# Performance work log

Measured on AMD Instinct MI355X. Metric: run time of the kernel, lower is better.

Reference implementation:

```python
import jax, jax.numpy as jnp
import numpy as np

B, T, D, H, L, INNER = 2, 2048, 1024, 16, 8, 4096
EPS = 1e-5
MASK_BIAS = -10000.0

def setup_inputs() -> dict:
    key = jax.random.key(0)
    ks = jax.random.split(key, 6)
    std = 0.02
    w = lambda k, shape: jax.random.normal(k, shape, jnp.float32) * std
    return {
        "inputs_embeds": jax.random.normal(ks[0], (B, T, D), jnp.float32),
        "attention_mask": jnp.ones((B, T), jnp.float32),
        "ln1_w": jnp.ones((L, D), jnp.float32), "ln1_b": jnp.zeros((L, D), jnp.float32),
        "attn_w": w(ks[1], (L, D, 3 * D)), "attn_b": jnp.zeros((L, 3 * D), jnp.float32),
        "proj_w": w(ks[2], (L, D, D)), "proj_b": jnp.zeros((L, D), jnp.float32),
        "ln2_w": jnp.ones((L, D), jnp.float32), "ln2_b": jnp.zeros((L, D), jnp.float32),
        "fc_w": w(ks[3], (L, D, INNER)), "fc_b": jnp.zeros((L, INNER), jnp.float32),
        "fcp_w": w(ks[4], (L, INNER, D)), "fcp_b": jnp.zeros((L, D), jnp.float32),
        "lnf_w": jnp.ones((D,), jnp.float32), "lnf_b": jnp.zeros((D,), jnp.float32),
    }

def _ln(x, w, b):
    m = jnp.mean(x, axis=-1, keepdims=True)
    v = jnp.var(x, axis=-1, keepdims=True)
    return (x - m) * jax.lax.rsqrt(v + EPS) * w + b

def reference(inputs_embeds, attention_mask, ln1_w, ln1_b, attn_w, attn_b,
              proj_w, proj_b, ln2_w, ln2_b, fc_w, fc_b, fcp_w, fcp_b,
              lnf_w, lnf_b):
    hd = D // H
    scale = 1.0 / np.sqrt(hd).astype(np.float32)
    causal = jnp.tril(jnp.ones((T, T), bool))            # [T,T]
    add_mask = (1.0 - attention_mask)[:, None, None, :] * MASK_BIAS  # [B,1,1,T]
    heads = lambda t: t.reshape(B, T, H, hd).transpose(0, 2, 1, 3)   # [B,H,T,hd]
    h = inputs_embeds  # dropout is identity at eval
    for i in range(L):
        # --- causal self-attention (manual QK^T / softmax / AV) ---
        x = _ln(h, ln1_w[i], ln1_b[i])
        qkv = x @ attn_w[i] + attn_b[i]                  # [B,T,3D]
        q, k, v = (heads(t) for t in jnp.split(qkv, 3, axis=-1))
        s = jnp.einsum('bhqd,bhkd->bhqk', q, k) * scale  # [B,H,T,T]
        s = jnp.where(causal, s, MASK_BIAS) + add_mask   # masked_fill then additive mask
        p = jax.nn.softmax(s, axis=-1)
        ctx = jnp.einsum('bhqk,bhkd->bhqd', p, v)
        ctx = ctx.transpose(0, 2, 1, 3).reshape(B, T, D)
        h = h + ctx @ proj_w[i] + proj_b[i]
        # --- feed-forward ---
        x = _ln(h, ln2_w[i], ln2_b[i])
        h = h + jax.nn.relu(x @ fc_w[i] + fc_b[i]) @ fcp_w[i] + fcp_b[i]
    return _ln(h, lnf_w, lnf_b)
```

## Files before the change

### kernel.cpp

```cpp
#include <hip/hip_runtime.h>
#include <math.h>

namespace {
constexpr int kB = 2;
constexpr int kT = 2048;
constexpr int kD = 1024;
constexpr int kH = 16;
constexpr int kL = 8;
constexpr int kInner = 4096;
constexpr int kM = kB * kT;
constexpr float kEps = 1e-5f;
}

typedef __attribute__((ext_vector_type(8))) short bf16x8;
typedef __attribute__((ext_vector_type(4))) float f32x4;
typedef __attribute__((ext_vector_type(16))) float f32x16;

typedef const __attribute__((address_space(1))) void* gas_t;
typedef __attribute__((address_space(3))) void* las_t;

__device__ __forceinline__ short f2bf(float f) {
  union { float f; unsigned u; } v{f};
  unsigned r = (v.u + 0x7FFF + ((v.u >> 16) & 1)) >> 16;
  return (short)r;
}

__device__ __forceinline__ unsigned cvtpk_bf16(float lo, float hi) {
  unsigned r;
  asm("v_cvt_pk_bf16_f32 %0, %1, %2" : "=v"(r) : "v"(lo), "v"(hi));
  return r;
}

__device__ __forceinline__ void half_swap(unsigned& a, unsigned& b, bool ishi) {
  const unsigned sel = ishi ? a : b;
  const unsigned got = (unsigned)__shfl_xor((int)sel, 32, 64);
  a = ishi ? got : a;
  b = ishi ? b : got;
}

template <typename OT>
__global__ __launch_bounds__(256) void ln_kernel(
    const float* __restrict__ in, const float* __restrict__ w,
    const float* __restrict__ b, OT* __restrict__ out) {
  const int row = blockIdx.x;
  const int tid = threadIdx.x;
  const float4 v = ((const float4*)(in + (size_t)row * kD))[tid];
  float sum = v.x + v.y + v.z + v.w;
  float sq = v.x * v.x + v.y * v.y + v.z * v.z + v.w * v.w;
#pragma unroll
  for (int off = 32; off > 0; off >>= 1) {
    sum += __shfl_down(sum, off);
    sq += __shfl_down(sq, off);
  }
  __shared__ float s1[4], s2[4];
  const int wave = tid >> 6, lane = tid & 63;
  if (lane == 0) { s1[wave] = sum; s2[wave] = sq; }
  __syncthreads();
  const float ts = s1[0] + s1[1] + s1[2] + s1[3];
  const float tq = s2[0] + s2[1] + s2[2] + s2[3];
  const float mean = ts * (1.0f / kD);
  const float var = tq * (1.0f / kD) - mean * mean;
  const float rs = rsqrtf(var + kEps);
  const float4 w4 = ((const float4*)w)[tid];
  const float4 b4 = ((const float4*)b)[tid];
  float4 o;
  o.x = (v.x - mean) * rs * w4.x + b4.x;
  o.y = (v.y - mean) * rs * w4.y + b4.y;
  o.z = (v.z - mean) * rs * w4.z + b4.z;
  o.w = (v.w - mean) * rs * w4.w + b4.w;
  if constexpr (sizeof(OT) == 4) {
    ((float4*)(out + (size_t)row * kD))[tid] = o;
  } else {
    short4 s4;
    s4.x = f2bf(o.x); s4.y = f2bf(o.y); s4.z = f2bf(o.z); s4.w = f2bf(o.w);
    ((short4*)(out + (size_t)row * kD))[tid] = s4;
  }
}

__global__ __launch_bounds__(256) void convT_kernel(
    const float* __restrict__ aw, const float* __restrict__ pw,
    const float* __restrict__ fw, const float* __restrict__ gw,
    short* __restrict__ awT, short* __restrict__ pwT,
    short* __restrict__ fwT, short* __restrict__ gwT) {
  __shared__ short t[64][66];
  int b = blockIdx.x;
  const float* src; short* dst; int K, N, tk, tn;
  if (b < 768)       { src = aw; dst = awT; K = 1024; N = 3072; tk = b / 48; tn = b % 48; }
  else if (b < 1024) { b -= 768;  src = pw; dst = pwT; K = 1024; N = 1024; tk = b / 16; tn = b % 16; }
  else if (b < 2048) { b -= 1024; src = fw; dst = fwT; K = 1024; N = 4096; tk = b / 64; tn = b % 64; }
  else               { b -= 2048; src = gw; dst = gwT; K = 4096; N = 1024; tk = b / 16; tn = b % 16; }
  const int k0 = tk * 64, n0 = tn * 64;
  const int tr = threadIdx.x >> 4, tc4 = (threadIdx.x & 15) << 2;
#pragma unroll
  for (int i = 0; i < 4; ++i) {
    const int k = tr + i * 16;
    const float4 v = *(const float4*)(src + (size_t)(k0 + k) * N + n0 + tc4);
    t[k][tc4 + 0] = f2bf(v.x); t[k][tc4 + 1] = f2bf(v.y);
    t[k][tc4 + 2] = f2bf(v.z); t[k][tc4 + 3] = f2bf(v.w);
  }
  __syncthreads();
#pragma unroll
  for (int i = 0; i < 4; ++i) {
    const int n = tr + i * 16;
    short4 o;
    o.x = t[tc4 + 0][n]; o.y = t[tc4 + 1][n];
    o.z = t[tc4 + 2][n]; o.w = t[tc4 + 3][n];
    *(short4*)(dst + (size_t)(n0 + n) * K + k0 + tc4) = o;
  }
}

template <int BN_, int OUT, bool RELU>
__global__ __launch_bounds__(256, 4) void mfma_gemm3(
    const short* __restrict__ A, const short* __restrict__ BT,
    const float* __restrict__ bias, const float* __restrict__ res,
    void* __restrict__ Cout, int N, int K) {
  constexpr int NJ = BN_ / 32;
  __shared__ __align__(16) short As[128 * 64];
  __shared__ __align__(16) short Bs[BN_ * 64];
  const int tid = threadIdx.x;
  const int w = tid >> 6, lane = tid & 63;
  const int n16 = lane & 15, quad = lane >> 4;
  const int gridN = N / BN_;
  int bid = blockIdx.x;
  const int nwg = gridDim.x;
  bid = (bid & 7) * (nwg >> 3) + (bid >> 3);
  const int m0 = (bid / gridN) * 128, n0 = (bid % gridN) * BN_;
  const int wr = (w >> 1) * 64, wc = (w & 1) * (BN_ / 2);

  const short* Ap = A + (size_t)m0 * K;
  const short* Bp = BT + (size_t)n0 * K;

  f32x4 acc[4][NJ];
#pragma unroll
  for (int i = 0; i < 4; ++i)
#pragma unroll
    for (int j = 0; j < NJ; ++j) acc[i][j] = (f32x4)0.f;

  const int srow = tid >> 3;
  const int schunk = tid & 7;

  for (int k0 = 0; k0 < K; k0 += 64) {
#pragma unroll
    for (int i = 0; i < 4; ++i) {
      const int r = i * 32 + srow;
      const int cs = (schunk ^ (r & 7)) << 3;
      __builtin_amdgcn_global_load_lds(
          (gas_t)(const void*)(Ap + (size_t)r * K + k0 + cs),
          (las_t)(void*)(As + (i * 32 + w * 8) * 64), 16, 0, 0);
      if (i < NJ)
        __builtin_amdgcn_global_load_lds(
            (gas_t)(const void*)(Bp + (size_t)r * K + k0 + cs),
            (las_t)(void*)(Bs + (i * 32 + w * 8) * 64), 16, 0, 0);
    }
    __syncthreads();

    bf16x8 af[4][2], bf[NJ][2];
#pragma unroll
    for (int i = 0; i < 4; ++i) {
      const int m = wr + i * 16 + n16;
#pragma unroll
      for (int kc = 0; kc < 2; ++kc)
        af[i][kc] =
            *(const bf16x8*)(As + m * 64 + ((((kc << 2) + quad) ^ (m & 7)) << 3));
    }
#pragma unroll
    for (int j = 0; j < NJ; ++j) {
      const int n = wc + j * 16 + n16;
#pragma unroll
      for (int kc = 0; kc < 2; ++kc)
        bf[j][kc] =
            *(const bf16x8*)(Bs + n * 64 + ((((kc << 2) + quad) ^ (n & 7)) << 3));
    }
#pragma unroll
    for (int i = 0; i < 4; ++i)
#pragma unroll
      for (int j = 0; j < NJ; ++j)
#pragma unroll
        for (int kc = 0; kc < 2; ++kc)
          acc[i][j] = __builtin_amdgcn_mfma_f32_16x16x32_bf16(af[i][kc], bf[j][kc],
                                                              acc[i][j], 0, 0, 0);
    __syncthreads();
  }

#pragma unroll
  for (int j = 0; j < NJ; ++j) {
    const int n = n0 + wc + j * 16 + n16;
    const float bv = bias[n];
#pragma unroll
    for (int i = 0; i < 4; ++i) {
#pragma unroll
      for (int r = 0; r < 4; ++r) {
        const int m = m0 + wr + i * 16 + quad * 4 + r;
        float v = acc[i][j][r] + bv;
        if (OUT == 1) {
          ((float*)Cout)[(size_t)m * N + n] = v + res[(size_t)m * N + n];
        } else {
          if (RELU) v = fmaxf(v, 0.f);
          ((short*)Cout)[(size_t)m * N + n] = f2bf(v);
        }
      }
    }
  }
}

__global__ __launch_bounds__(256) void attn_kernel(
    const short* __restrict__ qkv, const float* __restrict__ amaskp,
    short* __restrict__ ctx) {
  __shared__ __align__(16) short smem[2][8192];

  const int tid = threadIdx.x;
  const int w = tid >> 6;
  const int lane = tid & 63;
  const int l31 = lane & 31;
  const int hi = lane >> 5;
  const int bh = blockIdx.x;
  const int bb = bh >> 4, hh = bh & 15;
  const int qb = gridDim.y - 1 - blockIdx.y;
  const int q0 = qb * 128;
  const int qw0 = q0 + w * 32;

  const short* base  = qkv + (size_t)bb * kT * 3072;
  const short* kbase = base + 1024 + hh * 64;
  const short* vbase = base + 2048 + hh * 64;
  const float* amp   = amaskp + bb * kT;

  bf16x8 qf[4];
  {
    const short* qp = base + (size_t)(qw0 + l31) * 3072 + hh * 64 + hi * 8;
#pragma unroll
    for (int mi = 0; mi < 4; ++mi) qf[mi] = *(const bf16x8*)(qp + mi * 16);
  }

  f32x16 O[2];
  O[0] = (f32x16)0.f;
  O[1] = (f32x16)0.f;
  float m_r = -1e30f, l_r = 0.f;

  const int krow = tid >> 3, kch = tid & 7;
  const int vk4 = tid >> 5, vd16 = (tid >> 3) & 3;
  const int vkin = (tid >> 1) & 3, vdh = tid & 1;
  const int wuni = (tid & 192) * 8;

  const unsigned vs0 = (unsigned)(size_t)(las_t)(void*)(&smem[0][4096]);
  const int g = lane >> 4;
  const unsigned vtr =
      vs0 + (unsigned)((g >> 1) * 1024 + (g & 1) * 128 + (lane & 15) * 8);

  auto STAGE = [&](int buf, int k0) {
    short* ks = &smem[buf][0];
    short* vs = &smem[buf][4096];
#pragma unroll
    for (int r2 = 0; r2 < 2; ++r2) {
      const int rr = r2 * 32 + krow;
      __builtin_amdgcn_global_load_lds(
          (gas_t)(const void*)(kbase + (size_t)(k0 + rr) * 3072 +
                               ((kch ^ (rr & 7)) << 3)),
          (las_t)(void*)(ks + r2 * 2048 + wuni), 16, 0, 0);
      const int key = k0 + r2 * 32 + vk4 * 4 + vkin;
      __builtin_amdgcn_global_load_lds(
          (gas_t)(const void*)(vbase + (size_t)key * 3072 + vd16 * 16 + vdh * 8),
          (las_t)(void*)(vs + r2 * 2048 + wuni), 16, 0, 0);
    }
  };

  const int kend = q0 + 128;
  STAGE(0, 0);
  __syncthreads();
  int cur = 0;

  for (int k0 = 0; k0 < kend; k0 += 64) {
    if (k0 + 64 < kend) STAGE(cur ^ 1, k0 + 64);

    if (k0 <= qw0 + 31) {
      const short* ks = &smem[cur][0];

      f32x16 st[2];
      st[0] = (f32x16)0.f;
      st[1] = (f32x16)0.f;
#pragma unroll
      for (int s = 0; s < 2; ++s) {
        const int row = s * 32 + l31;
        const short* kp = ks + row * 64;
#pragma unroll
        for (int mi = 0; mi < 4; ++mi) {
          const bf16x8 kf =
              *(const bf16x8*)(kp + (((2 * mi + hi) ^ (row & 7)) << 3));
          st[s] = __builtin_amdgcn_mfma_f32_32x32x16_bf16(kf, qf[mi], st[s],
                                                          0, 0, 0);
        }
      }

#pragma unroll
      for (int s = 0; s < 2; ++s) {
        const bool pm = (k0 + 32 * s + 31 > qw0);
#pragma unroll
        for (int rq = 0; rq < 4; ++rq) {
          const int kb_ = k0 + 32 * s + 8 * rq + 4 * hi;
          const float4 a4 = *(const float4*)(amp + kb_);
          const float amv0 = (1.f - a4.x) * -10000.f;
          const float amv1 = (1.f - a4.y) * -10000.f;
          const float amv2 = (1.f - a4.z) * -10000.f;
          const float amv3 = (1.f - a4.w) * -10000.f;
          float v0 = st[s][rq * 4 + 0] * 0.125f;
          float v1 = st[s][rq * 4 + 1] * 0.125f;
          float v2 = st[s][rq * 4 + 2] * 0.125f;
          float v3 = st[s][rq * 4 + 3] * 0.125f;
          if (pm) {
            const int q = qw0 + l31;
            if (kb_ + 0 > q) v0 = -10000.f;
            if (kb_ + 1 > q) v1 = -10000.f;
            if (kb_ + 2 > q) v2 = -10000.f;
            if (kb_ + 3 > q) v3 = -10000.f;
          }
          st[s][rq * 4 + 0] = v0 + amv0;
          st[s][rq * 4 + 1] = v1 + amv1;
          st[s][rq * 4 + 2] = v2 + amv2;
          st[s][rq * 4 + 3] = v3 + amv3;
        }
      }

      float mx = st[0][0];
#pragma unroll
      for (int r = 1; r < 16; ++r) mx = fmaxf(mx, st[0][r]);
#pragma unroll
      for (int r = 0; r < 16; ++r) mx = fmaxf(mx, st[1][r]);
      mx = fmaxf(mx, __shfl_xor(mx, 32, 64));
      if (!__all(mx <= m_r + 8.f)) {
        const float mn = fmaxf(m_r, mx);
        const float al = __expf(m_r - mn);
        m_r = mn;
        l_r *= al;
#pragma unroll
        for (int r = 0; r < 16; ++r) {
          O[0][r] *= al;
          O[1][r] *= al;
        }
      }
      float sum = 0.f;
#pragma unroll
      for (int s = 0; s < 2; ++s)
#pragma unroll
        for (int r = 0; r < 16; ++r) {
          const float p = __expf(st[s][r] - m_r);
          st[s][r] = p;
          sum += p;
        }
      sum += __shfl_xor(sum, 32, 64);
      l_r += sum;

      bf16x8 pf[4];
      const bool ishi = (hi != 0);
#pragma unroll
      for (int s = 0; s < 2; ++s) {
#pragma unroll
        for (int hf = 0; hf < 2; ++hf) {
          unsigned wa = cvtpk_bf16(st[s][8 * hf + 0], st[s][8 * hf + 1]);
          unsigned wc = cvtpk_bf16(st[s][8 * hf + 4], st[s][8 * hf + 5]);
          half_swap(wa, wc, ishi);
          unsigned wb = cvtpk_bf16(st[s][8 * hf + 2], st[s][8 * hf + 3]);
          unsigned wd = cvtpk_bf16(st[s][8 * hf + 6], st[s][8 * hf + 7]);
          half_swap(wb, wd, ishi);
          union { unsigned u[4]; bf16x8 h; } f;
          f.u[0] = wa; f.u[1] = wb; f.u[2] = wc; f.u[3] = wd;
          pf[s * 2 + hf] = f.h;
        }
      }

      unsigned long long tv[16];
      const unsigned vb_ = vtr + (unsigned)(cur << 14);
#pragma unroll
      for (int c = 0; c < 4; ++c)
#pragma unroll
        for (int di = 0; di < 2; ++di) {
          asm volatile("ds_read_b64_tr_b16 %0, %1 offset:%2"
                       : "=v"(tv[(c * 2 + di) * 2 + 0])
                       : "v"(vb_), "n"(c * 2048 + di * 256));
          asm volatile("ds_read_b64_tr_b16 %0, %1 offset:%2"
                       : "=v"(tv[(c * 2 + di) * 2 + 1])
                       : "v"(vb_), "n"(c * 2048 + di * 256 + 512));
        }
      asm volatile("s_waitcnt lgkmcnt(0)" ::: "memory");
      __builtin_amdgcn_sched_barrier(0);
#pragma unroll
      for (int c = 0; c < 4; ++c)
#pragma unroll
        for (int di = 0; di < 2; ++di) {
          union { unsigned long long q[2]; bf16x8 h; } vf_;
          vf_.q[0] = tv[(c * 2 + di) * 2 + 0];
          vf_.q[1] = tv[(c * 2 + di) * 2 + 1];
          O[di] = __builtin_amdgcn_mfma_f32_32x32x16_bf16(vf_.h, pf[c], O[di],
                                                          0, 0, 0);
        }
    }

    __syncthreads();
    cur ^= 1;
  }

  const float inv = 1.f / l_r;
  const size_t tok = (size_t)bb * kT + qw0 + l31;
  short* cp = ctx + tok * 1024 + hh * 64 + 4 * hi;
#pragma unroll
  for (int di = 0; di < 2; ++di)
#pragma unroll
    for (int rq = 0; rq < 4; ++rq) {
      short4 o4;
      o4.x = f2bf(O[di][rq * 4 + 0] * inv);
      o4.y = f2bf(O[di][rq * 4 + 1] * inv);
      o4.z = f2bf(O[di][rq * 4 + 2] * inv);
      o4.w = f2bf(O[di][rq * 4 + 3] * inv);
      *(short4*)(cp + di * 32 + rq * 8) = o4;
    }
}

extern "C" void kernel_launch(void* const* d_in, const int* in_sizes, int n_in,
                              void* d_out, int out_size, void* d_ws, size_t ws_size,
                              hipStream_t stream) {
  const float* emb   = (const float*)d_in[0];
  const float* amask = (const float*)d_in[1];
  const float* ln1w  = (const float*)d_in[2];
  const float* ln1b  = (const float*)d_in[3];
  const float* attnw = (const float*)d_in[4];
  const float* attnb = (const float*)d_in[5];
  const float* projw = (const float*)d_in[6];
  const float* projb = (const float*)d_in[7];
  const float* ln2w  = (const float*)d_in[8];
  const float* ln2b  = (const float*)d_in[9];
  const float* fcw   = (const float*)d_in[10];
  const float* fcb   = (const float*)d_in[11];
  const float* fcpw  = (const float*)d_in[12];
  const float* fcpb  = (const float*)d_in[13];
  const float* lnfw  = (const float*)d_in[14];
  const float* lnfb  = (const float*)d_in[15];
  float* out = (float*)d_out;

  float* h    = (float*)d_ws;
  short* xb   = (short*)(h + (size_t)kM * kD);
  short* ctxb = xb + (size_t)kM * kD;
  short* bigb = ctxb + (size_t)kM * kD;
  short* awT  = bigb + (size_t)kM * kInner;
  short* pwT  = awT + (size_t)3072 * 1024;
  short* fwT  = pwT + (size_t)1024 * 1024;
  short* gwT  = fwT + (size_t)4096 * 1024;

  hipMemcpyAsync(h, emb, sizeof(float) * (size_t)kM * kD,
                 hipMemcpyDeviceToDevice, stream);

  const dim3 blk(256);
  for (int l = 0; l < kL; ++l) {
    convT_kernel<<<3072, blk, 0, stream>>>(
        attnw + (size_t)l * kD * 3072, projw + (size_t)l * kD * kD,
        fcw + (size_t)l * kD * kInner, fcpw + (size_t)l * kInner * kD,
        awT, pwT, fwT, gwT);
    ln_kernel<short><<<kM, blk, 0, stream>>>(h, ln1w + l * kD, ln1b + l * kD, xb);
    mfma_gemm3<128, 0, false><<<(3072 / 128) * (kM / 128), blk, 0, stream>>>(
        xb, awT, attnb + l * 3072, nullptr, bigb, 3072, 1024);
    attn_kernel<<<dim3(kB * kH, kT / 128), blk, 0, stream>>>(bigb, amask, ctxb);
    mfma_gemm3<64, 1, false><<<(1024 / 64) * (kM / 128), blk, 0, stream>>>(
        ctxb, pwT, projb + l * kD, h, h, 1024, 1024);
    ln_kernel<short><<<kM, blk, 0, stream>>>(h, ln2w + l * kD, ln2b + l * kD, xb);
    mfma_gemm3<128, 0, true><<<(4096 / 128) * (kM / 128), blk, 0, stream>>>(
        xb, fwT, fcb + l * kInner, nullptr, bigb, 4096, 1024);
    mfma_gemm3<64, 1, false><<<(1024 / 64) * (kM / 128), blk, 0, stream>>>(
        bigb, gwT, fcpb + l * kD, h, h, 1024, 4096);
  }
  ln_kernel<float><<<kM, blk, 0, stream>>>(h, lnfw, lnfb, out);
}
```

Baseline: 2.296 ms.

## Add 256x256 eight-wave pipelined GEMM for QKV and FC1 projections

Adds a new 512-thread GEMM kernel with 256x256 output tiles, double-buffered LDS filled by direct global-to-LDS loads, and a ping-pong schedule that interleaves quarter-tile MFMA blocks with staged loads, barriers and raised wave priority. It also applies an XCD-aware block-id remap so neighbouring tiles share L2. The kernel replaces the 128-tile GEMM for the QKV and FC1 projections, aiming for more data reuse per loaded tile and better overlap of loads with compute. In exchange the grid for these GEMMs shrinks to 192 and 256 blocks, which may underfill the GPU, and the kernel needs heavy register and LDS use.

```diff
diff --git a/kernel.cpp b/kernel.cpp
--- a/kernel.cpp
+++ b/kernel.cpp
@@ -203,6 +203,144 @@
   }
 }
 
+template <bool RELU>
+__global__ __launch_bounds__(512, 2) void mfma_gemm8(
+    const short* __restrict__ A, const short* __restrict__ BT,
+    const float* __restrict__ bias, short* __restrict__ Cout, int N, int K) {
+  __shared__ __align__(16) short As[2][2][128 * 64];
+  __shared__ __align__(16) short Bs[2][2][128 * 64];
+  const int tid = threadIdx.x;
+  const int w = tid >> 6, lane = tid & 63;
+  const int n16 = lane & 15, quad = lane >> 4;
+  const int wm = w >> 2, wn = w & 3;
+  const int gridN = N >> 8;
+  int bid = blockIdx.x;
+  const int nwg = gridDim.x;
+  bid = (bid & 7) * (nwg >> 3) + (bid >> 3);
+  const int m0 = (bid / gridN) * 256, n0 = (bid % gridN) * 256;
+  const short* Ap = A + (size_t)m0 * K;
+  const short* Bp = BT + (size_t)n0 * K;
+
+  f32x4 acc[8][4];
+#pragma unroll
+  for (int i = 0; i < 8; ++i)
+#pragma unroll
+    for (int j = 0; j < 4; ++j) acc[i][j] = (f32x4)0.f;
+
+  const int srow = tid >> 3;
+  const int schunk = tid & 7;
+
+  auto STAGEH = [&](const short* P, short* dst, int half, int kk) {
+#pragma unroll
+    for (int r = 0; r < 2; ++r) {
+      const int row = r * 64 + srow;
+      __builtin_amdgcn_global_load_lds(
+          (gas_t)(const void*)(P + (size_t)(half * 128 + row) * K + kk +
+                               ((schunk ^ (row & 7)) << 3)),
+          (las_t)(void*)(dst + (r * 64 + w * 8) * 64), 16, 0, 0);
+    }
+  };
+
+  bf16x8 afA[4][2], afB[4][2], bf[2][2];
+  auto LDA = [&](bf16x8 (&af)[4][2], const short* ash, int qm) {
+#pragma unroll
+    for (int mi = 0; mi < 4; ++mi) {
+      const int row = qm * 64 + mi * 16 + n16;
+#pragma unroll
+      for (int kc = 0; kc < 2; ++kc)
+        af[mi][kc] = *(const bf16x8*)(ash + row * 64 +
+                                      ((((kc << 2) + quad) ^ (row & 7)) << 3));
+    }
+  };
+  auto LDB = [&](const short* bsw, int qn) {
+#pragma unroll
+    for (int nj = 0; nj < 2; ++nj) {
+      const int row = qn * 32 + nj * 16 + n16;
+#pragma unroll
+      for (int kc = 0; kc < 2; ++kc)
+        bf[nj][kc] = *(const bf16x8*)(bsw + row * 64 +
+                                      ((((kc << 2) + quad) ^ (row & 7)) << 3));
+    }
+  };
+
+#define MMQ(AF, QM, QN)                                                       \
+  {                                                                           \
+    __builtin_amdgcn_s_setprio(1);                                            \
+    _Pragma("unroll") for (int mi = 0; mi < 4; ++mi)                          \
+    _Pragma("unroll") for (int nj = 0; nj < 2; ++nj)                          \
+    _Pragma("unroll") for (int kc = 0; kc < 2; ++kc)                          \
+        acc[(QM)*4 + mi][(QN)*2 + nj] =                                       \
+            __builtin_amdgcn_mfma_f32_16x16x32_bf16(                          \
+                AF[mi][kc], bf[nj][kc], acc[(QM)*4 + mi][(QN)*2 + nj],        \
+                0, 0, 0);                                                     \
+    __builtin_amdgcn_s_setprio(0);                                            \
+  }
+
+  const int NT = K >> 6;
+  STAGEH(Ap, &As[0][0][0], 0, 0);
+  STAGEH(Ap, &As[0][1][0], 1, 0);
+  STAGEH(Bp, &Bs[0][0][0], 0, 0);
+  STAGEH(Bp, &Bs[0][1][0], 1, 0);
+  STAGEH(Ap, &As[1][0][0], 0, 64);
+  STAGEH(Ap, &As[1][1][0], 1, 64);
+  asm volatile("s_waitcnt vmcnt(4)" ::: "memory");
+  __builtin_amdgcn_s_barrier();
+
+  for (int t = 0; t < NT; ++t) {
+    const int buf = t & 1, ob = buf ^ 1;
+    const short* aw = &As[buf][wm][0];
+    const short* bw = &Bs[buf][wn >> 1][(wn & 1) * 64 * 64];
+    const int kn1 = (t + 1) << 6, kn2 = (t + 2) << 6;
+    const bool s1 = (t + 1) < NT, s2 = (t + 2) < NT;
+
+    LDA(afA, aw, 0);
+    LDB(bw, 0);
+    if (s1) STAGEH(Bp, &Bs[ob][0][0], 0, kn1);
+    __builtin_amdgcn_s_barrier();
+    MMQ(afA, 0, 0);
+    __builtin_amdgcn_s_barrier();
+
+    LDA(afB, aw, 1);
+    if (s1) STAGEH(Bp, &Bs[ob][1][0], 1, kn1);
+    __builtin_amdgcn_s_barrier();
+    MMQ(afB, 1, 0);
+    __builtin_amdgcn_s_barrier();
+
+    LDB(bw, 1);
+    if (s2) STAGEH(Ap, &As[buf][0][0], 0, kn2);
+    __builtin_amdgcn_s_barrier();
+    MMQ(afA, 0, 1);
+    __builtin_amdgcn_s_barrier();
+
+    if (s2) {
+      STAGEH(Ap, &As[buf][1][0], 1, kn2);
+      asm volatile("s_waitcnt vmcnt(4)" ::: "memory");
+    } else {
+      asm volatile("s_waitcnt vmcnt(0)" ::: "memory");
+    }
+    __builtin_amdgcn_s_barrier();
+    MMQ(afB, 1, 1);
+    __builtin_amdgcn_s_barrier();
+  }
+#undef MMQ
+
+#pragma unroll
+  for (int j = 0; j < 4; ++j) {
+    const int n = n0 + wn * 64 + (j >> 1) * 32 + (j & 1) * 16 + n16;
+    const float bv = bias[n];
+#pragma unroll
+    for (int i = 0; i < 8; ++i) {
+#pragma unroll
+      for (int r = 0; r < 4; ++r) {
+        const int m = m0 + wm * 128 + (i >> 2) * 64 + (i & 3) * 16 + quad * 4 + r;
+        float v = acc[i][j][r] + bv;
+        if (RELU) v = fmaxf(v, 0.f);
+        Cout[(size_t)m * N + n] = f2bf(v);
+      }
+    }
+  }
+}
+
 __global__ __launch_bounds__(256) void attn_kernel(
     const short* __restrict__ qkv, const float* __restrict__ amaskp,
     short* __restrict__ ctx) {
@@ -447,20 +585,21 @@
                  hipMemcpyDeviceToDevice, stream);
 
   const dim3 blk(256);
+  const dim3 blk512(512);
   for (int l = 0; l < kL; ++l) {
     convT_kernel<<<3072, blk, 0, stream>>>(
         attnw + (size_t)l * kD * 3072, projw + (size_t)l * kD * kD,
         fcw + (size_t)l * kD * kInner, fcpw + (size_t)l * kInner * kD,
         awT, pwT, fwT, gwT);
     ln_kernel<short><<<kM, blk, 0, stream>>>(h, ln1w + l * kD, ln1b + l * kD, xb);
-    mfma_gemm3<128, 0, false><<<(3072 / 128) * (kM / 128), blk, 0, stream>>>(
-        xb, awT, attnb + l * 3072, nullptr, bigb, 3072, 1024);
+    mfma_gemm8<false><<<(3072 / 256) * (kM / 256), blk512, 0, stream>>>(
+        xb, awT, attnb + l * 3072, bigb, 3072, 1024);
     attn_kernel<<<dim3(kB * kH, kT / 128), blk, 0, stream>>>(bigb, amask, ctxb);
     mfma_gemm3<64, 1, false><<<(1024 / 64) * (kM / 128), blk, 0, stream>>>(
         ctxb, pwT, projb + l * kD, h, h, 1024, 1024);
     ln_kernel<short><<<kM, blk, 0, stream>>>(h, ln2w + l * kD, ln2b + l * kD, xb);
-    mfma_gemm3<128, 0, true><<<(4096 / 128) * (kM / 128), blk, 0, stream>>>(
-        xb, fwT, fcb + l * kInner, nullptr, bigb, 4096, 1024);
+    mfma_gemm8<true><<<(4096 / 256) * (kM / 256), blk512, 0, stream>>>(
+        xb, fwT, fcb + l * kInner, bigb, 4096, 1024);
     mfma_gemm3<64, 1, false><<<(1024 / 64) * (kM / 128), blk, 0, stream>>>(
         bigb, gwT, fcpb + l * kD, h, h, 1024, 4096);
   }
```

Measured after the change: 2.268 ms. Within noise of the previous version (-1.2%).
